# Kernel tuning notes

Hardware: AMD Instinct MI355X
Metric: run time of the kernel (lower is better)

Reference implementation:

```python
import jax, jax.numpy as jnp
import numpy as np


def setup_inputs() -> dict:
    key = jax.random.key(0)
    k1, k2, k3 = jax.random.split(key, 3)
    B, C, D, H, W = 4, 64, 32, 64, 64
    K = 32
    X = jax.random.normal(k1, (B, C, D, H, W), dtype=jnp.float32)
    std1 = 1.0 / float(np.sqrt(K * C))
    codewords = jax.random.uniform(k2, (K, C), minval=-std1, maxval=std1, dtype=jnp.float32)
    scale = jax.random.uniform(k3, (K,), minval=-1.0, maxval=0.0, dtype=jnp.float32)
    return {"X": X, "codewords": codewords, "scale": scale}


def reference(X, codewords, scale):
    B, C, D, H, W = X.shape
    K = codewords.shape[0]
    N = D * H * W
    # (B, N, C) feature view
    Xf = jnp.transpose(X.reshape(B, C, N), (0, 2, 1))
    X2 = jnp.sum(Xf * Xf, axis=-1, keepdims=True)          # (B, N, 1)
    C2 = jnp.sum(codewords * codewords, axis=-1)            # (K,)
    XC = jnp.einsum('bnc,kc->bnk', Xf, codewords)           # (B, N, K)
    logits = scale * (X2 + C2 - 2.0 * XC)
    A = jax.nn.softmax(logits, axis=2)                      # (B, N, K)
    # coefA: (B, K, D, H, W); dropout is identity in eval mode
    coefA = jnp.transpose(A, (0, 2, 1)).reshape(B, K, D, H, W)
    # aggregate: E[b,k,:] = sum_n A[b,n,k]*(X[b,n,:]-C[k,:])
    # algebraic rewrite: A^T @ X - (sum_n A) * C   (avoids (B,N,K,C) blowup)
    AtX = jnp.einsum('bnk,bnc->bkc', A, Xf)                 # (B, K, C)
    Asum = jnp.sum(A, axis=1)                               # (B, K)
    E = AtX - Asum[..., None] * codewords[None, :, :]
    return (E, coefA)
```

## Files before the change

kernel.cpp:

```cpp
#include <hip/hip_runtime.h>
#include <hip/hip_bf16.h>

typedef short short8 __attribute__((ext_vector_type(8)));
typedef float f32x4  __attribute__((ext_vector_type(4)));

#define BB      4
#define CC      64
#define KK      32
#define NN      131072
#define TILE    128
#define NTILE   1024
#define JBLK    192
#define THREADS 256
#define PSZ     2080

#define XN_S 72
#define XC_S 136
#define AK_S 136

__device__ __forceinline__ void barrier_lds() {
    __builtin_amdgcn_s_waitcnt(0xC07F);
    __builtin_amdgcn_s_barrier();
}

__device__ __forceinline__ unsigned pk2(float a, float b) {
    union { __hip_bfloat162 h; unsigned u; } cv;
    cv.h = __float22bfloat162_rn(make_float2(a, b));
    return cv.u;
}
__device__ __forceinline__ unsigned short b16(float a) {
    union { __hip_bfloat16 h; unsigned short u; } cv;
    cv.h = __float2bfloat16(a);
    return cv.u;
}

__global__ __launch_bounds__(THREADS, 3) void main_kernel(
        const float* __restrict__ X,
        const float* __restrict__ cw,
        const float* __restrict__ scale,
        float* __restrict__ out,
        float* __restrict__ ws) {
    __shared__ __align__(16) unsigned short Xn[TILE][XN_S];
    __shared__ __align__(16) unsigned short Xc[CC][XC_S];
    __shared__ __align__(16) unsigned short Ak[KK][AK_S];
    __shared__ float x2l[2][TILE];
    __shared__ float asml[4][KK];

    const int tid  = threadIdx.x;
    const int b    = blockIdx.x / JBLK;
    const int j    = blockIdx.x % JBLK;
    const int lane = tid & 63;
    const int w    = tid >> 6;
    const int q    = lane >> 4;
    const int l15  = lane & 15;

    const float* Xb   = X + (size_t)b * CC * NN;
    float*       outA = out + 8192 + (size_t)b * KK * NN;

    short8 cwf[2][2];
    float c2acc[2] = {0.f, 0.f};
    #pragma unroll
    for (int kt = 0; kt < 2; ++kt)
        #pragma unroll
        for (int s = 0; s < 2; ++s) {
            const float* cp = cw + (16 * kt + l15) * CC + 32 * s + 8 * q;
            #pragma unroll
            for (int jj = 0; jj < 8; ++jj) {
                float v = cp[jj];
                c2acc[kt] += v * v;
                cwf[kt][s][jj] = (short)b16(v);
            }
        }
    #pragma unroll
    for (int kt = 0; kt < 2; ++kt) {
        c2acc[kt] += __shfl_xor(c2acc[kt], 16);
        c2acc[kt] += __shfl_xor(c2acc[kt], 32);
    }
    float s2v[2][4], sc2v[2][4], sclv[2][4];
    #pragma unroll
    for (int t2 = 0; t2 < 2; ++t2)
        #pragma unroll
        for (int r = 0; r < 4; ++r) {
            int k = 16 * t2 + 4 * q + r;
            float sk  = scale[k];
            float c2k = __shfl(c2acc[t2], 4 * q + r);
            sclv[t2][r] = sk;
            s2v[t2][r]  = -2.0f * sk;
            sc2v[t2][r] = sk * c2k;
        }

    const f32x4 zf = {0.f, 0.f, 0.f, 0.f};
    f32x4 acc2[2] = {zf, zf};
    float asum[2][4];
    #pragma unroll
    for (int t2 = 0; t2 < 2; ++t2)
        #pragma unroll
        for (int r = 0; r < 4; ++r) asum[t2][r] = 0.f;

    const int n1 = tid & 127, ch = tid >> 7;
    const int kt2 = w & 1, ct0 = (w >> 1) * 2;

    float xv[32];
    {
        const float* p1 = Xb + (size_t)(32 * ch) * NN + (size_t)j * TILE + n1;
        #pragma unroll
        for (int i = 0; i < 32; ++i) xv[i] = p1[(size_t)i * NN];
    }

    for (int t = j; t < NTILE; t += JBLK) {
        const size_t nb = (size_t)t * TILE;

        float x2 = 0.f;
        #pragma unroll
        for (int i = 0; i < 32; ++i) x2 += xv[i] * xv[i];
        x2l[ch][n1] = x2;
        #pragma unroll
        for (int g = 0; g < 4; ++g) {
            uint4 u;
            u.x = pk2(xv[8*g+0], xv[8*g+1]); u.y = pk2(xv[8*g+2], xv[8*g+3]);
            u.z = pk2(xv[8*g+4], xv[8*g+5]); u.w = pk2(xv[8*g+6], xv[8*g+7]);
            *(uint4*)&Xn[n1][32 * ch + 8 * g] = u;
        }
        #pragma unroll
        for (int i = 0; i < 32; ++i)
            Xc[32 * ch + i][n1] = b16(xv[i]);

        barrier_lds();

        const int tn = t + JBLK;
        float xn[32];
        if (tn < NTILE) {
            const float* pn = Xb + (size_t)(32 * ch) * NN + (size_t)tn * TILE + n1;
            #pragma unroll
            for (int i = 0; i < 32; ++i) xn[i] = pn[(size_t)i * NN];
        }

        #pragma unroll
        for (int nt = 2 * w; nt < 2 * w + 2; ++nt) {
            const int nl = nt * 16 + l15;
            const float x2n = x2l[0][nl] + x2l[1][nl];
            short8 bx0 = *(const short8*)&Xn[nl][8 * q];
            short8 bx1 = *(const short8*)&Xn[nl][32 + 8 * q];
            f32x4 lt[2];
            lt[0] = __builtin_amdgcn_mfma_f32_16x16x32_bf16(cwf[0][0], bx0, zf, 0, 0, 0);
            lt[0] = __builtin_amdgcn_mfma_f32_16x16x32_bf16(cwf[0][1], bx1, lt[0], 0, 0, 0);
            lt[1] = __builtin_amdgcn_mfma_f32_16x16x32_bf16(cwf[1][0], bx0, zf, 0, 0, 0);
            lt[1] = __builtin_amdgcn_mfma_f32_16x16x32_bf16(cwf[1][1], bx1, lt[1], 0, 0, 0);

            float av[2][4];
            float m = -3.0e38f;
            #pragma unroll
            for (int t2 = 0; t2 < 2; ++t2)
                #pragma unroll
                for (int r = 0; r < 4; ++r) {
                    float L = fmaf(s2v[t2][r], lt[t2][r],
                                   fmaf(sclv[t2][r], x2n, sc2v[t2][r]));
                    av[t2][r] = L;
                    m = fmaxf(m, L);
                }
            m = fmaxf(m, __shfl_xor(m, 16));
            m = fmaxf(m, __shfl_xor(m, 32));
            float s = 0.f;
            #pragma unroll
            for (int t2 = 0; t2 < 2; ++t2)
                #pragma unroll
                for (int r = 0; r < 4; ++r) {
                    float e = __expf(av[t2][r] - m);
                    av[t2][r] = e;
                    s += e;
                }
            s += __shfl_xor(s, 16);
            s += __shfl_xor(s, 32);
            const float inv = 1.0f / s;
            #pragma unroll
            for (int t2 = 0; t2 < 2; ++t2)
                #pragma unroll
                for (int r = 0; r < 4; ++r) {
                    float a = av[t2][r] * inv;
                    int k = 16 * t2 + 4 * q + r;
                    asum[t2][r] += a;
                    outA[(size_t)k * NN + nb + nl] = a;
                    Ak[k][nl] = b16(a);
                }
        }

        barrier_lds();

        #pragma unroll
        for (int s = 0; s < 4; ++s) {
            short8 af  = *(const short8*)&Ak[16 * kt2 + l15][32 * s + 8 * q];
            short8 bc0 = *(const short8*)&Xc[16 * ct0 + l15][32 * s + 8 * q];
            short8 bc1 = *(const short8*)&Xc[16 * (ct0 + 1) + l15][32 * s + 8 * q];
            acc2[0] = __builtin_amdgcn_mfma_f32_16x16x32_bf16(af, bc0, acc2[0], 0, 0, 0);
            acc2[1] = __builtin_amdgcn_mfma_f32_16x16x32_bf16(af, bc1, acc2[1], 0, 0, 0);
        }

        barrier_lds();

        if (tn < NTILE) {
            #pragma unroll
            for (int i = 0; i < 32; ++i) xv[i] = xn[i];
        }
    }

    float* p = ws + (size_t)blockIdx.x * PSZ;
    #pragma unroll
    for (int cti = 0; cti < 2; ++cti)
        #pragma unroll
        for (int r = 0; r < 4; ++r) {
            int k = 16 * kt2 + 4 * q + r;
            int c = 16 * (ct0 + cti) + l15;
            p[k * CC + c] = acc2[cti][r];
        }
    #pragma unroll
    for (int t2 = 0; t2 < 2; ++t2)
        #pragma unroll
        for (int r = 0; r < 4; ++r) {
            float v = asum[t2][r];
            v += __shfl_xor(v, 1); v += __shfl_xor(v, 2);
            v += __shfl_xor(v, 4); v += __shfl_xor(v, 8);
            if (l15 == 0) asml[w][16 * t2 + 4 * q + r] = v;
        }
    barrier_lds();
    if (tid < KK)
        p[2048 + tid] = asml[0][tid] + asml[1][tid] + asml[2][tid] + asml[3][tid];
}

__global__ __launch_bounds__(256) void finalize_kernel(
        const float* __restrict__ cw,
        float* __restrict__ out,
        const float* __restrict__ ws) {
    __shared__ float red[4][64];
    __shared__ float ar[192];
    const int b = blockIdx.x >> 5;
    const int k = blockIdx.x & 31;
    const int c  = threadIdx.x & 63;
    const int jg = threadIdx.x >> 6;

    const float* p0 = ws + (size_t)b * JBLK * PSZ;
    float atx = 0.f;
    for (int j2 = jg; j2 < JBLK; j2 += 4)
        atx += p0[(size_t)j2 * PSZ + k * CC + c];
    red[jg][c] = atx;
    if (threadIdx.x < 192)
        ar[threadIdx.x] = p0[(size_t)threadIdx.x * PSZ + 2048 + k];
    __syncthreads();
    if (threadIdx.x < 64) {
        float a = red[0][c] + red[1][c] + red[2][c] + red[3][c];
        float s = ar[c] + ar[c + 64] + ar[c + 128];
        s += __shfl_xor(s, 1);  s += __shfl_xor(s, 2);  s += __shfl_xor(s, 4);
        s += __shfl_xor(s, 8);  s += __shfl_xor(s, 16); s += __shfl_xor(s, 32);
        out[(size_t)(b * KK + k) * CC + c] = a - s * cw[k * CC + c];
    }
}

extern "C" void kernel_launch(void* const* d_in, const int* in_sizes, int n_in,
                              void* d_out, int out_size, void* d_ws, size_t ws_size,
                              hipStream_t stream) {
    const float* X  = (const float*)d_in[0];
    const float* cw = (const float*)d_in[1];
    const float* sc = (const float*)d_in[2];
    float* out = (float*)d_out;
    float* ws  = (float*)d_ws;

    main_kernel<<<BB * JBLK, THREADS, 0, stream>>>(X, cw, sc, out, ws);
    finalize_kernel<<<BB * KK, 256, 0, stream>>>(cw, out, ws);
}
```

Before: 240.0 us.

## Make each wave own a 32-column subtile to drop block-wide barriers

```diff
diff --git a/kernel.cpp b/kernel.cpp
--- a/kernel.cpp
+++ b/kernel.cpp
@@ -3,6 +3,8 @@
 
 typedef short short8 __attribute__((ext_vector_type(8)));
 typedef float f32x4  __attribute__((ext_vector_type(4)));
+typedef unsigned int u32x4 __attribute__((ext_vector_type(4)));
+typedef unsigned int u32x2 __attribute__((ext_vector_type(2)));
 
 #define BB      4
 #define CC      64
@@ -15,12 +17,22 @@
 #define PSZ     2080
 
 #define XN_S 72
-#define XC_S 136
-#define AK_S 136
-
-__device__ __forceinline__ void barrier_lds() {
-    __builtin_amdgcn_s_waitcnt(0xC07F);
-    __builtin_amdgcn_s_barrier();
+#define XC_S 40
+#define AK_S 40
+
+struct Tiles {
+    unsigned short Xn[4][32][XN_S];
+    unsigned short Xc[4][64][XC_S];
+    unsigned short Ak[4][32][AK_S];
+};
+union SMem {
+    Tiles t;
+    float red[4][2048];
+};
+
+__device__ __forceinline__ void wave_sync() {
+    asm volatile("s_waitcnt lgkmcnt(0)" ::: "memory");
+    __builtin_amdgcn_sched_barrier(0);
 }
 
 __device__ __forceinline__ unsigned pk2(float a, float b) {
@@ -40,10 +52,7 @@
         const float* __restrict__ scale,
         float* __restrict__ out,
         float* __restrict__ ws) {
-    __shared__ __align__(16) unsigned short Xn[TILE][XN_S];
-    __shared__ __align__(16) unsigned short Xc[CC][XC_S];
-    __shared__ __align__(16) unsigned short Ak[KK][AK_S];
-    __shared__ float x2l[2][TILE];
+    __shared__ __align__(16) SMem sm;
     __shared__ float asml[4][KK];
 
     const int tid  = threadIdx.x;
@@ -53,9 +62,15 @@
     const int w    = tid >> 6;
     const int q    = lane >> 4;
     const int l15  = lane & 15;
+    const int nq   = lane & 7;
+    const int co   = lane >> 3;
 
     const float* Xb   = X + (size_t)b * CC * NN;
     float*       outA = out + 8192 + (size_t)b * KK * NN;
+
+    unsigned short (*Xn)[XN_S] = sm.t.Xn[w];
+    unsigned short (*Xc)[XC_S] = sm.t.Xc[w];
+    unsigned short (*Ak)[AK_S] = sm.t.Ak[w];
 
     short8 cwf[2][2];
     float c2acc[2] = {0.f, 0.f};
@@ -90,55 +105,71 @@
         }
 
     const f32x4 zf = {0.f, 0.f, 0.f, 0.f};
-    f32x4 acc2[2] = {zf, zf};
+    f32x4 acc2[2][4];
+    #pragma unroll
+    for (int kt = 0; kt < 2; ++kt)
+        #pragma unroll
+        for (int ct = 0; ct < 4; ++ct) acc2[kt][ct] = zf;
     float asum[2][4];
     #pragma unroll
     for (int t2 = 0; t2 < 2; ++t2)
         #pragma unroll
         for (int r = 0; r < 4; ++r) asum[t2][r] = 0.f;
 
-    const int n1 = tid & 127, ch = tid >> 7;
-    const int kt2 = w & 1, ct0 = (w >> 1) * 2;
-
-    float xv[32];
-    {
-        const float* p1 = Xb + (size_t)(32 * ch) * NN + (size_t)j * TILE + n1;
-        #pragma unroll
-        for (int i = 0; i < 32; ++i) xv[i] = p1[(size_t)i * NN];
-    }
-
     for (int t = j; t < NTILE; t += JBLK) {
-        const size_t nb = (size_t)t * TILE;
-
-        float x2 = 0.f;
-        #pragma unroll
-        for (int i = 0; i < 32; ++i) x2 += xv[i] * xv[i];
-        x2l[ch][n1] = x2;
-        #pragma unroll
-        for (int g = 0; g < 4; ++g) {
-            uint4 u;
-            u.x = pk2(xv[8*g+0], xv[8*g+1]); u.y = pk2(xv[8*g+2], xv[8*g+3]);
-            u.z = pk2(xv[8*g+4], xv[8*g+5]); u.w = pk2(xv[8*g+6], xv[8*g+7]);
-            *(uint4*)&Xn[n1][32 * ch + 8 * g] = u;
-        }
-        #pragma unroll
-        for (int i = 0; i < 32; ++i)
-            Xc[32 * ch + i][n1] = b16(xv[i]);
-
-        barrier_lds();
-
-        const int tn = t + JBLK;
-        float xn[32];
-        if (tn < NTILE) {
-            const float* pn = Xb + (size_t)(32 * ch) * NN + (size_t)tn * TILE + n1;
-            #pragma unroll
-            for (int i = 0; i < 32; ++i) xn[i] = pn[(size_t)i * NN];
-        }
-
-        #pragma unroll
-        for (int nt = 2 * w; nt < 2 * w + 2; ++nt) {
-            const int nl = nt * 16 + l15;
-            const float x2n = x2l[0][nl] + x2l[1][nl];
+        const size_t n0 = (size_t)t * TILE + 32 * w;
+
+        const float* pb = Xb + (size_t)(8 * co) * NN + n0 + 4 * nq;
+        f32x4 xv[8];
+        #pragma unroll
+        for (int i = 0; i < 8; ++i)
+            xv[i] = *(const f32x4*)(pb + (size_t)i * NN);
+
+        float xp[4] = {0.f, 0.f, 0.f, 0.f};
+        #pragma unroll
+        for (int i = 0; i < 8; ++i) {
+            xp[0] = fmaf(xv[i][0], xv[i][0], xp[0]);
+            xp[1] = fmaf(xv[i][1], xv[i][1], xp[1]);
+            xp[2] = fmaf(xv[i][2], xv[i][2], xp[2]);
+            xp[3] = fmaf(xv[i][3], xv[i][3], xp[3]);
+        }
+        #pragma unroll
+        for (int dn = 0; dn < 4; ++dn) {
+            u32x4 u;
+            u[0] = pk2(xv[0][dn], xv[1][dn]);
+            u[1] = pk2(xv[2][dn], xv[3][dn]);
+            u[2] = pk2(xv[4][dn], xv[5][dn]);
+            u[3] = pk2(xv[6][dn], xv[7][dn]);
+            *(u32x4*)&Xn[4 * nq + dn][8 * co] = u;
+        }
+        #pragma unroll
+        for (int i = 0; i < 8; ++i) {
+            u32x2 u;
+            u[0] = pk2(xv[i][0], xv[i][1]);
+            u[1] = pk2(xv[i][2], xv[i][3]);
+            *(u32x2*)&Xc[8 * co + i][4 * nq] = u;
+        }
+        #pragma unroll
+        for (int d = 0; d < 4; ++d) {
+            xp[d] += __shfl_xor(xp[d], 8);
+            xp[d] += __shfl_xor(xp[d], 16);
+            xp[d] += __shfl_xor(xp[d], 32);
+        }
+
+        wave_sync();
+
+        #pragma unroll
+        for (int nt = 0; nt < 2; ++nt) {
+            const int nl  = nt * 16 + l15;
+            const int src = 4 * nt + (l15 >> 2);
+            float xs0 = __shfl(xp[0], src);
+            float xs1 = __shfl(xp[1], src);
+            float xs2 = __shfl(xp[2], src);
+            float xs3 = __shfl(xp[3], src);
+            float xa  = (l15 & 1) ? xs1 : xs0;
+            float xb2 = (l15 & 1) ? xs3 : xs2;
+            float x2n = (l15 & 2) ? xb2 : xa;
+
             short8 bx0 = *(const short8*)&Xn[nl][8 * q];
             short8 bx1 = *(const short8*)&Xn[nl][32 + 8 * q];
             f32x4 lt[2];
@@ -179,39 +210,35 @@
                     float a = av[t2][r] * inv;
                     int k = 16 * t2 + 4 * q + r;
                     asum[t2][r] += a;
-                    outA[(size_t)k * NN + nb + nl] = a;
+                    outA[(size_t)k * NN + n0 + nl] = a;
                     Ak[k][nl] = b16(a);
                 }
         }
 
-        barrier_lds();
-
-        #pragma unroll
-        for (int s = 0; s < 4; ++s) {
-            short8 af  = *(const short8*)&Ak[16 * kt2 + l15][32 * s + 8 * q];
-            short8 bc0 = *(const short8*)&Xc[16 * ct0 + l15][32 * s + 8 * q];
-            short8 bc1 = *(const short8*)&Xc[16 * (ct0 + 1) + l15][32 * s + 8 * q];
-            acc2[0] = __builtin_amdgcn_mfma_f32_16x16x32_bf16(af, bc0, acc2[0], 0, 0, 0);
-            acc2[1] = __builtin_amdgcn_mfma_f32_16x16x32_bf16(af, bc1, acc2[1], 0, 0, 0);
-        }
-
-        barrier_lds();
-
-        if (tn < NTILE) {
-            #pragma unroll
-            for (int i = 0; i < 32; ++i) xv[i] = xn[i];
-        }
+        wave_sync();
+
+        short8 af0 = *(const short8*)&Ak[l15][8 * q];
+        short8 af1 = *(const short8*)&Ak[16 + l15][8 * q];
+        #pragma unroll
+        for (int ct = 0; ct < 4; ++ct) {
+            short8 bc = *(const short8*)&Xc[16 * ct + l15][8 * q];
+            acc2[0][ct] = __builtin_amdgcn_mfma_f32_16x16x32_bf16(af0, bc, acc2[0][ct], 0, 0, 0);
+            acc2[1][ct] = __builtin_amdgcn_mfma_f32_16x16x32_bf16(af1, bc, acc2[1][ct], 0, 0, 0);
+        }
+        __builtin_amdgcn_sched_barrier(0);
     }
 
-    float* p = ws + (size_t)blockIdx.x * PSZ;
-    #pragma unroll
-    for (int cti = 0; cti < 2; ++cti)
-        #pragma unroll
-        for (int r = 0; r < 4; ++r) {
-            int k = 16 * kt2 + 4 * q + r;
-            int c = 16 * (ct0 + cti) + l15;
-            p[k * CC + c] = acc2[cti][r];
-        }
+    __syncthreads();
+    #pragma unroll
+    for (int kt = 0; kt < 2; ++kt)
+        #pragma unroll
+        for (int ct = 0; ct < 4; ++ct)
+            #pragma unroll
+            for (int r = 0; r < 4; ++r) {
+                int k = 16 * kt + 4 * q + r;
+                int c = 16 * ct + l15;
+                sm.red[w][k * CC + c] = acc2[kt][ct][r];
+            }
     #pragma unroll
     for (int t2 = 0; t2 < 2; ++t2)
         #pragma unroll
@@ -221,7 +248,13 @@
             v += __shfl_xor(v, 4); v += __shfl_xor(v, 8);
             if (l15 == 0) asml[w][16 * t2 + 4 * q + r] = v;
         }
-    barrier_lds();
+    __syncthreads();
+    float* p = ws + (size_t)blockIdx.x * PSZ;
+    #pragma unroll
+    for (int i = 0; i < 8; ++i) {
+        int idx = tid + 256 * i;
+        p[idx] = sm.red[0][idx] + sm.red[1][idx] + sm.red[2][idx] + sm.red[3][idx];
+    }
     if (tid < KK)
         p[2048 + tid] = asml[0][tid] + asml[1][tid] + asml[2][tid] + asml[3][tid];
 }
```

Result: slower. 247.6 us (+3.2%).
